# Kernel tuning notes

Measured on AMD Instinct MI355X. Metric: run time of the kernel, lower is better.

The kernel has to match this reference:

```python
import jax, jax.numpy as jnp
import numpy as np

DT = 1.0
S = 64            # num_sites
D = 2 * S         # state_dim
LOG_2PI = float(np.log(2.0 * np.pi))

def _selectors():
    s0 = np.zeros((2, 4), np.float32); s0[:, 0:2] = np.eye(2)
    s1 = np.zeros((2, 4), np.float32); s1[:, 2:4] = np.eye(2)
    cr = 0.5 * (s0 + s1)
    # [target=2, source=2, 2, 4]; off-diagonal pairs use the averaged selector
    return jnp.asarray(np.stack([np.stack([s0, cr]), np.stack([cr, s1])]))

SEL = _selectors()

def project_lon_lat(lon, lat):
    # lon, lat: [B,S]
    lat0 = lat.mean(-1, keepdims=True)
    lon0 = lon.mean(-1, keepdims=True)
    km = 111.32
    x = (lon - lon0) * (km * jnp.cos(jnp.deg2rad(lat0)))
    y = (lat - lat0) * km
    coords = jnp.stack([x, y], -1)                        # [B,S,2]
    h = coords[:, :, None, :] - coords[:, None, :, :]
    dist = jnp.sqrt((h ** 2).sum(-1) + 1e-12)
    npos = (dist > 1e-6).sum((-1, -2)).astype(coords.dtype)
    scale = dist.sum((-1, -2)) / jnp.maximum(npos, 1.0)
    return coords / jnp.maximum(scale, 1e-6)[:, None, None]

def build_A(h, mu, sigma, coupling, damping, eyeD):
    # h: [B,S,S,2], mu: [B,4], sigma: [B,4,4]
    B = mu.shape[0]
    sigma = 0.5 * (sigma + jnp.swapaxes(sigma, -1, -2))
    dm = jnp.einsum('tsab,nb->tsna', SEL, mu)                     # [2,2,B,2]
    dc = jnp.einsum('tsab,nbc,tsdc->tsnad', SEL, sigma, SEL)      # [2,2,B,2,2]
    dc = 0.5 * (dc + jnp.swapaxes(dc, -1, -2))
    eye2 = jnp.eye(2, dtype=h.dtype)
    Dm = (1.0 + 1e-4) * eye2 + (2.0 * DT ** 2) * dc
    Dinv = jnp.linalg.inv(Dm)
    _, logdet = jnp.linalg.slogdet(Dm)
    diff = h[None, None] - DT * dm[:, :, :, None, None, :]        # [2,2,B,S,S,2]
    q = jnp.einsum('tsbijd,tsbdf,tsbijf->tsbij', diff, Dinv, diff)
    ker = jnp.exp(-0.5 * (q + logdet[..., None, None]))
    ker = ker / jnp.maximum(ker.sum(-1, keepdims=True), 1e-6)
    ker = jnp.moveaxis(ker, 2, 0)                                 # [B,2,2,S,S]
    op = ker * coupling[None, :, :, None, None]
    op = jnp.transpose(op, (0, 1, 3, 2, 4)).reshape(B, D, D)
    return eyeD + DT * (op - damping * eyeD)

def _update(m, P, z_t, r2, eyeD):
    # Kalman measurement update with H = I, R = r2*I; returns per-sample NLL term
    Sm = P + r2 * eyeD
    v = z_t - m
    Sinv_v = jnp.linalg.solve(Sm, v[..., None])[..., 0]
    _, logdet = jnp.linalg.slogdet(Sm)
    nll_t = 0.5 * ((v * Sinv_v).sum(-1) + logdet + D * LOG_2PI)
    K = jnp.swapaxes(jnp.linalg.solve(Sm, P), -1, -2)   # P @ Sm^{-1} (P, Sm symmetric)
    m = m + jnp.einsum('bij,bj->bi', K, v)
    P = jnp.einsum('bij,bjk->bik', eyeD - K, P)
    return m, P, nll_t

def reference(z_seq, site_lon, site_lat, mu_seq, sigma_seq,
              log_q_proc, log_r_obs, log_p0, log_damping,
              init_mean, coupling_raw):
    B, T = z_seq.shape[0], z_seq.shape[1]
    z = z_seq.reshape(B, T, D)
    dtype = z.dtype
    eyeD = jnp.eye(D, dtype=dtype)
    r2 = jnp.exp(log_r_obs) ** 2
    q2 = jnp.exp(log_q_proc) ** 2
    damping = jnp.exp(log_damping)
    coupling = jnp.eye(2, dtype=dtype) + 0.25 * jnp.tanh(coupling_raw)

    lon = jnp.broadcast_to(site_lon[None], (B, S))
    lat = jnp.broadcast_to(site_lat[None], (B, S))
    coords = project_lon_lat(lon, lat)
    h = coords[:, :, None, :] - coords[:, None, :, :]   # [B,S,S,2]

    m0 = jnp.broadcast_to(init_mean[None], (B, D))
    P0 = jnp.broadcast_to(jnp.exp(log_p0) ** 2 * eyeD, (B, D, D))
    m, P, nll0 = _update(m0, P0, z[:, 0], r2, eyeD)

    def step(carry, xs):
        m, P = carry
        mu_t, sigma_t, z_t = xs
        A = build_A(h, mu_t, sigma_t, coupling, damping, eyeD)
        m = jnp.einsum('bij,bj->bi', A, m)
        P = jnp.einsum('bij,bjk,blk->bil', A, P, A) + q2 * eyeD
        m, P, nll_t = _update(m, P, z_t, r2, eyeD)
        return (m, P), nll_t

    xs = (jnp.swapaxes(mu_seq, 0, 1), jnp.swapaxes(sigma_seq, 0, 1),
          jnp.swapaxes(z[:, 1:], 0, 1))
    (_, _), nll_rest = jax.lax.scan(step, (m, P), xs)
    nll = nll0 + nll_rest.sum(0)   # [B]
    return nll.mean()

def setup_inputs() -> dict:
    key = jax.random.key(0)
    ks = jax.random.split(key, 5)
    B, T = 16, 128
    z_seq = jax.random.normal(ks[0], (B, T, S, 2), jnp.float32)
    site_lon = 10.0 + 0.5 * jax.random.uniform(ks[1], (S,), jnp.float32)
    site_lat = 55.0 + 0.5 * jax.random.uniform(ks[2], (S,), jnp.float32)
    mu_seq = 0.5 * jax.random.normal(ks[3], (B, T - 1, 4), jnp.float32)
    L = 0.2 * jax.random.normal(ks[4], (B, T - 1, 4, 4), jnp.float32)
    sigma_seq = jnp.einsum('btij,btkj->btik', L, L)   # PSD covariances
    return {
        'z_seq': z_seq, 'site_lon': site_lon, 'site_lat': site_lat,
        'mu_seq': mu_seq, 'sigma_seq': sigma_seq,
        'log_q_proc': jnp.float32(-2.0), 'log_r_obs': jnp.float32(-2.0),
        'log_p0': jnp.float32(0.0), 'log_damping': jnp.float32(0.0),
        'init_mean': jnp.zeros((D,), jnp.float32),
        'coupling_raw': jnp.zeros((2, 2), jnp.float32),
    }
```

## Files before the change

### kernel.cpp

```cpp
#include <hip/hip_runtime.h>
#include <math.h>


#define SQ 64
#define DQ 128
#define TQ 128
#define BQ 16
#define LDP 132
#define LDB 136
#define WFLOATS 17408
#define NTH 1024
#define LOG2PI 1.8378770664093454f

#define SMEM_FLOATS 35472

typedef __attribute__((ext_vector_type(8))) short bf16x8;
typedef __attribute__((ext_vector_type(4))) float f32x4;

__device__ __forceinline__ void lds_fence() {
  __asm__ volatile("s_waitcnt lgkmcnt(0)" ::: "memory");
}

__device__ __forceinline__ unsigned short f2bf(float f) {
  unsigned u = __float_as_uint(f);
  u += 0x7fffu + ((u >> 16) & 1u);
  return (unsigned short)(u >> 16);
}
__device__ __forceinline__ uint4 pack8(const float* v) {
  uint4 r;
  r.x = (unsigned)f2bf(v[0]) | ((unsigned)f2bf(v[1]) << 16);
  r.y = (unsigned)f2bf(v[2]) | ((unsigned)f2bf(v[3]) << 16);
  r.z = (unsigned)f2bf(v[4]) | ((unsigned)f2bf(v[5]) << 16);
  r.w = (unsigned)f2bf(v[6]) | ((unsigned)f2bf(v[7]) << 16);
  return r;
}

__device__ __forceinline__ float block_reduce_sum(float v, float* red) {
  #pragma unroll
  for (int off = 32; off > 0; off >>= 1) v += __shfl_down(v, off);
  const int tid = threadIdx.x;
  if ((tid & 63) == 0) red[tid >> 6] = v;
  __syncthreads();
  v = 0.0f;
  #pragma unroll
  for (int w = 0; w < NTH / 64; w++) v += red[w];
  __syncthreads();
  return v;
}

__device__ __forceinline__ void chol16_f(float* __restrict__ Wf,
                                         float* __restrict__ mdiag,
                                         int b0, int lane) {
  float a[16];
  if (lane < 16) {
    const float4* rp = (const float4*)(Wf + (b0 + lane) * LDP + b0);
    float4 q0 = rp[0], q1 = rp[1], q2v = rp[2], q3 = rp[3];
    a[0]=q0.x; a[1]=q0.y; a[2]=q0.z; a[3]=q0.w;
    a[4]=q1.x; a[5]=q1.y; a[6]=q1.z; a[7]=q1.w;
    a[8]=q2v.x; a[9]=q2v.y; a[10]=q2v.z; a[11]=q2v.w;
    a[12]=q3.x; a[13]=q3.y; a[14]=q3.z; a[15]=q3.w;
  } else {
    #pragma unroll
    for (int i = 0; i < 16; i++) a[i] = 1.0f;
  }
  float myrinv = 1.0f;
  #pragma unroll
  for (int j = 0; j < 16; j++) {
    float dj = __shfl(a[j], j);
    float rinv = rsqrtf(dj);
    float lij = a[j] * rinv;
    a[j] = lij;
    if (lane == j) myrinv = rinv;
    #pragma unroll
    for (int k = j + 1; k < 16; k++) {
      float lkj = __shfl(lij, k);
      a[k] = fmaf(-lij, lkj, a[k]);
    }
  }
  if (lane < 16) {
    float4* rp = (float4*)(Wf + (b0 + lane) * LDP + b0);
    rp[0] = make_float4(a[0], a[1], a[2], a[3]);
    rp[1] = make_float4(a[4], a[5], a[6], a[7]);
    rp[2] = make_float4(a[8], a[9], a[10], a[11]);
    rp[3] = make_float4(a[12], a[13], a[14], a[15]);
    mdiag[b0 + lane] = myrinv;
  }
}

__device__ __forceinline__ void trinv_chain2(float* __restrict__ Wf,
                                             const float* __restrict__ mdiag,
                                             int J, int pass, int lane,
                                             bool do1) {
  const int c16 = lane & 15;
  const int j16 = 4 * (lane >> 4) + pass;
  const int sh = lane & 48;
  if (do1) {
    float row[16];
    const float4* rp = (const float4*)(Wf + (J * 16 + c16) * LDP + J * 16);
    float4 a0 = rp[0], a1 = rp[1], a2 = rp[2], a3 = rp[3];
    row[0]=a0.x; row[1]=a0.y; row[2]=a0.z; row[3]=a0.w;
    row[4]=a1.x; row[5]=a1.y; row[6]=a1.z; row[7]=a1.w;
    row[8]=a2.x; row[9]=a2.y; row[10]=a2.z; row[11]=a2.w;
    row[12]=a3.x; row[13]=a3.y; row[14]=a3.z; row[15]=a3.w;
    float s = (c16 == j16) ? 1.0f : 0.0f;
    #pragma unroll
    for (int k = 0; k < 16; k++) {
      if (c16 == k) s *= mdiag[J * 16 + k];
      float sk = __shfl(s, sh | k);
      if (c16 > k) s = fmaf(-row[k], sk, s);
    }
    if (c16 > j16) Wf[(J * 16 + j16) * LDP + (J * 16 + c16)] = s;
    lds_fence();
  }
  const float md = mdiag[J * 16 + j16];
  const float* Mrow = Wf + (J * 16 + j16) * LDP + J * 16;
  #pragma unroll 1
  for (int I = J + 1; I < 8; I++) {
    const float* Lrow = Wf + (I * 16 + c16) * LDP + J * 16;
    float g = 0.0f;
    #pragma unroll
    for (int c4 = 0; c4 < 4; c4++) {
      float4 lv = *(const float4*)&Lrow[c4 * 4];
      float4 mq = *(const float4*)&Mrow[c4 * 4];
      float w0 = (c4*4+0 > j16) ? mq.x : ((c4*4+0 == j16) ? md : 0.0f);
      float w1 = (c4*4+1 > j16) ? mq.y : ((c4*4+1 == j16) ? md : 0.0f);
      float w2 = (c4*4+2 > j16) ? mq.z : ((c4*4+2 == j16) ? md : 0.0f);
      float w3 = (c4*4+3 > j16) ? mq.w : ((c4*4+3 == j16) ? md : 0.0f);
      g = fmaf(lv.x, w0, g); g = fmaf(lv.y, w1, g);
      g = fmaf(lv.z, w2, g); g = fmaf(lv.w, w3, g);
    }
    for (int K = J + 1; K < I; K++) {
      const float* LK = Lrow + (K - J) * 16;
      const float* MK = Wf + (J * 16 + j16) * LDP + K * 16;
      #pragma unroll
      for (int c4 = 0; c4 < 4; c4++) {
        float4 lv = *(const float4*)&LK[c4 * 4];
        float4 mq = *(const float4*)&MK[c4 * 4];
        g = fmaf(lv.x, mq.x, g); g = fmaf(lv.y, mq.y, g);
        g = fmaf(lv.z, mq.z, g); g = fmaf(lv.w, mq.w, g);
      }
    }
    if (I < 7) {
      float s = mdiag[I * 16 + c16] * g;
      #pragma unroll
      for (int k = 0; k < 15; k++) {
        float gk = __shfl(g, sh | k);
        if (k < c16) {
          float u = Wf[(I * 16 + k) * LDP + I * 16 + c16];
          s = fmaf(u, gk, s);
        }
      }
      Wf[(J * 16 + j16) * LDP + (I * 16 + c16)] = -s;
    } else {
      float row2[16];
      {
        const float4* rp2 = (const float4*)(Wf + (I * 16 + c16) * LDP + I * 16);
        float4 a0 = rp2[0], a1 = rp2[1], a2 = rp2[2], a3 = rp2[3];
        row2[0]=a0.x; row2[1]=a0.y; row2[2]=a0.z; row2[3]=a0.w;
        row2[4]=a1.x; row2[5]=a1.y; row2[6]=a1.z; row2[7]=a1.w;
        row2[8]=a2.x; row2[9]=a2.y; row2[10]=a2.z; row2[11]=a2.w;
        row2[12]=a3.x; row2[13]=a3.y; row2[14]=a3.z; row2[15]=a3.w;
      }
      float sv = g;
      #pragma unroll
      for (int k = 0; k < 16; k++) {
        if (c16 == k) sv *= mdiag[I * 16 + k];
        float sk = __shfl(sv, sh | k);
        if (c16 > k) sv = fmaf(-row2[k], sk, sv);
      }
      Wf[(J * 16 + j16) * LDP + (I * 16 + c16)] = -sv;
    }
    lds_fence();
  }
}

extern "C" __global__ __launch_bounds__(NTH, 4)
void ide_kf_kernel(const float* __restrict__ z_seq,
                   const float* __restrict__ site_lon,
                   const float* __restrict__ site_lat,
                   const float* __restrict__ mu_seq,
                   const float* __restrict__ sigma_seq,
                   const float* __restrict__ log_q,
                   const float* __restrict__ log_r,
                   const float* __restrict__ log_p0,
                   const float* __restrict__ log_damp,
                   const float* __restrict__ init_mean,
                   const float* __restrict__ coupling_raw,
                   float* __restrict__ ws) {
  extern __shared__ float smem[];
  float* Wf     = smem;
  float* B1f    = Wf + WFLOATS;
  float* B2f    = B1f + 8704;
  float* coords = B2f + 8704;
  float* mv     = coords + 128;
  float* vv     = mv + DQ;
  float* yv     = vv + DQ;
  float* mdiag  = yv + DQ;
  float* red    = mdiag + DQ;

  unsigned short* Tb  = (unsigned short*)Wf;
  unsigned short* Ab2 = (unsigned short*)Wf + 17408;
  unsigned short* Mtb = (unsigned short*)B1f;
  unsigned short* Pb  = (unsigned short*)B2f;
  unsigned short* Lhi = (unsigned short*)B1f;
  unsigned short* Llo = (unsigned short*)B2f;

  const int tid = threadIdx.x;
  const int lane = tid & 63;
  const int wave = tid >> 6;
  const int rb = wave >> 1, ch = wave & 1;
  const int m16 = lane & 15, quad = lane >> 4;
  const int grp = wave >> 2, pass = wave & 3;
  const int b = blockIdx.x;
  float* nll_out = ws;

  const float r2 = __expf(2.0f * log_r[0]);
  const float q2 = __expf(2.0f * log_q[0]);
  const float p0sq = __expf(2.0f * log_p0[0]);
  const float damping = __expf(log_damp[0]);
  const float cpl00 = 1.0f + 0.25f * tanhf(coupling_raw[0]);
  const float cpl01 = 0.25f * tanhf(coupling_raw[1]);
  const float cpl10 = 0.25f * tanhf(coupling_raw[2]);
  const float cpl11 = 1.0f + 0.25f * tanhf(coupling_raw[3]);

  float myLon = (tid < SQ) ? site_lon[tid] : 0.0f;
  float myLat = (tid < SQ) ? site_lat[tid] : 0.0f;
  float lat0 = block_reduce_sum(myLat, red) * (1.0f / 64.0f);
  float lon0 = block_reduce_sum(myLon, red) * (1.0f / 64.0f);
  if (tid < SQ) {
    const float km = 111.32f;
    float cs = cosf(lat0 * 0.017453292519943295f);
    coords[2 * tid]     = (myLon - lon0) * (km * cs);
    coords[2 * tid + 1] = (myLat - lat0) * km;
  }
  __syncthreads();
  float dsum = 0.0f, dcnt = 0.0f;
  for (int idx = tid; idx < SQ * SQ; idx += NTH) {
    int i = idx >> 6, j = idx & 63;
    float dx = coords[2 * i] - coords[2 * j];
    float dy = coords[2 * i + 1] - coords[2 * j + 1];
    float d = sqrtf(dx * dx + dy * dy + 1e-12f);
    dsum += d;
    if (d > 1e-6f) dcnt += 1.0f;
  }
  dsum = block_reduce_sum(dsum, red);
  dcnt = block_reduce_sum(dcnt, red);
  float scale = dsum / fmaxf(dcnt, 1.0f);
  float sdiv = 1.0f / fmaxf(scale, 1e-6f);
  if (tid < SQ) { coords[2 * tid] *= sdiv; coords[2 * tid + 1] *= sdiv; }

  for (int e = tid; e < WFLOATS / 4; e += NTH)
    ((float4*)Wf)[e] = make_float4(0.0f, 0.0f, 0.0f, 0.0f);
  for (int e = tid; e < 8704 / 4; e += NTH)
    ((float4*)B2f)[e] = make_float4(0.0f, 0.0f, 0.0f, 0.0f);
  __syncthreads();
  if (tid < DQ) {
    Wf[tid * LDP + tid] = p0sq + r2;
    mv[tid] = init_mean[tid];
  }
  __syncthreads();

  float nllp = 0.0f;

  #pragma unroll 1
  for (int t = 0; t < TQ; t++) {
    const float* zt = z_seq + ((size_t)b * TQ + t) * DQ;

    if (t > 0) {
      {
        f32x4 acc[4];
        #pragma unroll
        for (int c = 0; c < 4; c++) acc[c] = (f32x4){0.0f, 0.0f, 0.0f, 0.0f};
        #pragma unroll
        for (int ks = 0; ks < 4; ks++) {
          const int ko = 32 * ks + 8 * quad;
          bf16x8 a = *(const bf16x8*)(Ab2 + (16 * rb + m16) * LDB + ko);
          #pragma unroll
          for (int ct = 0; ct < 4; ct++) {
            bf16x8 bb = *(const bf16x8*)(Pb + (64 * ch + 16 * ct + m16) * LDB + ko);
            acc[ct] = __builtin_amdgcn_mfma_f32_16x16x32_bf16(a, bb, acc[ct], 0, 0, 0);
          }
        }
        #pragma unroll
        for (int ct = 0; ct < 4; ct++)
          #pragma unroll
          for (int reg = 0; reg < 4; reg++)
            Tb[(16 * rb + 4 * quad + reg) * LDB + 64 * ch + 16 * ct + m16] =
                f2bf(acc[ct][reg]);
        __syncthreads();
      }

      {
        const int ctmax = rb - 4 * ch;
        f32x4 acc[4];
        #pragma unroll
        for (int c = 0; c < 4; c++) acc[c] = (f32x4){0.0f, 0.0f, 0.0f, 0.0f};
        const bool gemv_wave = (wave == 1 || wave == 3);
        const int grow = (wave == 1) ? lane : 64 + lane;
        float newm = 0.0f;
        if (ctmax >= 0) {
          #pragma unroll
          for (int ks = 0; ks < 4; ks++) {
            const int ko = 32 * ks + 8 * quad;
            bf16x8 a = *(const bf16x8*)(Tb + (16 * rb + m16) * LDB + ko);
            #pragma unroll
            for (int ct = 0; ct < 4; ct++) {
              if (ct <= ctmax) {
                bf16x8 bb = *(const bf16x8*)(Ab2 + (64 * ch + 16 * ct + m16) * LDB + ko);
                acc[ct] = __builtin_amdgcn_mfma_f32_16x16x32_bf16(a, bb, acc[ct], 0, 0, 0);
              }
            }
          }
        } else if (gemv_wave) {
          const unsigned* ar = (const unsigned*)(Ab2 + grow * LDB);
          #pragma unroll 8
          for (int k2 = 0; k2 < 64; k2++) {
            unsigned p = ar[k2];
            newm = fmaf(__uint_as_float(p << 16), mv[2 * k2], newm);
            newm = fmaf(__uint_as_float(p & 0xffff0000u), mv[2 * k2 + 1], newm);
          }
        }
        __syncthreads();
        if (ctmax >= 0) {
          #pragma unroll
          for (int ct = 0; ct < 4; ct++) {
            if (ct <= ctmax) {
              #pragma unroll
              for (int reg = 0; reg < 4; reg++) {
                const int rg = 16 * rb + 4 * quad + reg;
                const int cgl = 64 * ch + 16 * ct + m16;
                Wf[rg * LDP + cgl] = acc[ct][reg] + ((rg == cgl) ? (q2 + r2) : 0.0f);
              }
            }
          }
        }
        if (gemv_wave) vv[grow] = zt[grow] - newm;
        if (wave == 0) {
          lds_fence();
          chol16_f(Wf, mdiag, 0, lane);
        }
        __syncthreads();
      }
    }

    if (t == 0) {
      if (tid < 64) {
        chol16_f(Wf, mdiag, 0, lane);
      } else if (tid < 192) {
        const int i = tid - 64;
        vv[i] = zt[i] - mv[i];
      }
      __syncthreads();
    }

    #pragma unroll 1
    for (int kb = 0; kb < 7; kb++) {
      const int b0k = kb * 16, base = b0k + 16, nbelow = DQ - base;
      if (tid < nbelow) {
        const int r = base + tid;
        float* wr = Wf + r * LDP + b0k;
        float w[16];
        #pragma unroll
        for (int u4 = 0; u4 < 4; u4++) {
          float4 w4 = *(const float4*)&wr[u4 * 4];
          w[u4*4] = w4.x; w[u4*4+1] = w4.y; w[u4*4+2] = w4.z; w[u4*4+3] = w4.w;
        }
        #pragma unroll
        for (int j = 0; j < 16; j++) {
          float s = w[j];
          #pragma unroll
          for (int l = 0; l < 16; l++) {
            if (l < j) s = fmaf(-w[l], Wf[(b0k + j) * LDP + b0k + l], s);
          }
          w[j] = s * mdiag[b0k + j];
        }
        #pragma unroll
        for (int u4 = 0; u4 < 4; u4++)
          *(float4*)&wr[u4 * 4] =
              make_float4(w[u4*4], w[u4*4+1], w[u4*4+2], w[u4*4+3]);
        unsigned short hs[16]; float lo[16];
        #pragma unroll
        for (int u = 0; u < 16; u++) {
          hs[u] = f2bf(w[u]);
          lo[u] = w[u] - __uint_as_float(((unsigned)hs[u]) << 16);
        }
        uint4 h0, h1;
        h0.x = hs[0] | ((unsigned)hs[1] << 16);   h0.y = hs[2] | ((unsigned)hs[3] << 16);
        h0.z = hs[4] | ((unsigned)hs[5] << 16);   h0.w = hs[6] | ((unsigned)hs[7] << 16);
        h1.x = hs[8] | ((unsigned)hs[9] << 16);   h1.y = hs[10] | ((unsigned)hs[11] << 16);
        h1.z = hs[12] | ((unsigned)hs[13] << 16); h1.w = hs[14] | ((unsigned)hs[15] << 16);
        unsigned short* hr = Lhi + r * LDB + b0k;
        unsigned short* lr = Llo + r * LDB + b0k;
        *(uint4*)(hr) = h0; *(uint4*)(hr + 8) = h1;
        *(uint4*)(lr) = pack8(lo); *(uint4*)(lr + 8) = pack8(lo + 8);
        const uint4 z4 = make_uint4(0u, 0u, 0u, 0u);
        *(uint4*)(hr + 16) = z4; *(uint4*)(hr + 24) = z4;
        *(uint4*)(lr + 16) = z4; *(uint4*)(lr + 24) = z4;
      }
      __syncthreads();
      if (wave <= 6 - kb) {
        const int bi = kb + 1 + wave;
        const int nch = (kb + 2) >> 1;
        f32x4 acc = (f32x4){0.0f, 0.0f, 0.0f, 0.0f};
        for (int c = 0; c < nch; c++) {
          const int ko = 32 * c + 8 * quad;
          bf16x8 ahi = *(const bf16x8*)(Lhi + (16 * bi + m16) * LDB + ko);
          bf16x8 alo = *(const bf16x8*)(Llo + (16 * bi + m16) * LDB + ko);
          bf16x8 bhi = *(const bf16x8*)(Lhi + (base + m16) * LDB + ko);
          bf16x8 blo = *(const bf16x8*)(Llo + (base + m16) * LDB + ko);
          acc = __builtin_amdgcn_mfma_f32_16x16x32_bf16(ahi, bhi, acc, 0, 0, 0);
          acc = __builtin_amdgcn_mfma_f32_16x16x32_bf16(ahi, blo, acc, 0, 0, 0);
          acc = __builtin_amdgcn_mfma_f32_16x16x32_bf16(alo, bhi, acc, 0, 0, 0);
        }
        #pragma unroll
        for (int reg = 0; reg < 4; reg++)
          Wf[(16 * bi + 4 * quad + reg) * LDP + base + m16] -= acc[reg];
        if (wave == 0) {
          lds_fence();
          chol16_f(Wf, mdiag, base, lane);
        }
      } else if (wave >= 8 && wave <= 11) {
        const int c16 = lane & 15;
        const int j16s = 4 * (lane >> 4) + (wave - 8);
        const int sh = lane & 48;
        float row[16];
        const float4* rp = (const float4*)(Wf + (b0k + c16) * LDP + b0k);
        float4 a0 = rp[0], a1 = rp[1], a2 = rp[2], a3 = rp[3];
        row[0]=a0.x; row[1]=a0.y; row[2]=a0.z; row[3]=a0.w;
        row[4]=a1.x; row[5]=a1.y; row[6]=a1.z; row[7]=a1.w;
        row[8]=a2.x; row[9]=a2.y; row[10]=a2.z; row[11]=a2.w;
        row[12]=a3.x; row[13]=a3.y; row[14]=a3.z; row[15]=a3.w;
        float s = (c16 == j16s) ? 1.0f : 0.0f;
        #pragma unroll
        for (int k = 0; k < 16; k++) {
          if (c16 == k) s *= mdiag[b0k + k];
          float sk = __shfl(s, sh | k);
          if (c16 > k) s = fmaf(-row[k], sk, s);
        }
        if (c16 > j16s) Wf[(b0k + j16s) * LDP + (b0k + c16)] = s;
      }
      __syncthreads();
    }

    {
      #pragma unroll 1
      for (int cc = 0; cc < 2; cc++) {
        const int J = cc ? (7 - grp) : grp;
        trinv_chain2(Wf, mdiag, J, pass, lane, cc == 1 && grp == 0);
      }
      __syncthreads();
    }

    {
      const int mrow = tid >> 3, kc = (tid & 7) * 16;
      float mtv[16];
      if (kc > mrow) {
        const float4* rp = (const float4*)(Wf + mrow * LDP + kc);
        float4 q0 = rp[0], q1 = rp[1], q2v = rp[2], q3 = rp[3];
        mtv[0]=q0.x; mtv[1]=q0.y; mtv[2]=q0.z; mtv[3]=q0.w;
        mtv[4]=q1.x; mtv[5]=q1.y; mtv[6]=q1.z; mtv[7]=q1.w;
        mtv[8]=q2v.x; mtv[9]=q2v.y; mtv[10]=q2v.z; mtv[11]=q2v.w;
        mtv[12]=q3.x; mtv[13]=q3.y; mtv[14]=q3.z; mtv[15]=q3.w;
      } else if (kc + 15 < mrow) {
        #pragma unroll
        for (int u = 0; u < 16; u++) mtv[u] = 0.0f;
      } else {
        #pragma unroll
        for (int u = 0; u < 16; u++) {
          const int k = kc + u;
          mtv[u] = (k > mrow) ? Wf[mrow * LDP + k]
                 : ((k == mrow) ? mdiag[mrow] : 0.0f);
        }
      }
      if (tid < DQ) {
        nllp -= __logf(mdiag[tid]);
        float s = mdiag[tid] * vv[tid];
        for (int k = 0; k < tid; k++) s = fmaf(Wf[k * LDP + tid], vv[k], s);
        yv[tid] = s;
      }
      unsigned short* mt = Mtb + mrow * LDB + kc;
      *(uint4*)(mt) = pack8(mtv);
      *(uint4*)(mt + 8) = pack8(mtv + 8);
      __syncthreads();
    }

    {
      f32x4 acc[4];
      #pragma unroll
      for (int c = 0; c < 4; c++) acc[c] = (f32x4){0.0f, 0.0f, 0.0f, 0.0f};
      if (tid < DQ) nllp += 0.5f * yv[tid] * yv[tid];
      const int ctmax = rb - 4 * ch;
      if (ctmax >= 0) {
        for (int ks = (rb >> 1); ks < 4; ks++) {
          const int ko = 32 * ks + 8 * quad;
          bf16x8 a = *(const bf16x8*)(Mtb + (16 * rb + m16) * LDB + ko);
          #pragma unroll
          for (int ct = 0; ct < 4; ct++) {
            if (ct <= ctmax) {
              bf16x8 bb = *(const bf16x8*)(Mtb + (64 * ch + 16 * ct + m16) * LDB + ko);
              acc[ct] = __builtin_amdgcn_mfma_f32_16x16x32_bf16(a, bb, acc[ct], 0, 0, 0);
            }
          }
        }
      }
      const float nr22 = -r2 * r2;
      #pragma unroll
      for (int ct = 0; ct < 4; ct++) {
        if (ct <= ctmax) {
          const bool strict = (ct < ctmax);
          #pragma unroll
          for (int reg = 0; reg < 4; reg++) {
            const int rg = 16 * rb + 4 * quad + reg;
            const int cgl = 64 * ch + 16 * ct + m16;
            unsigned short hv = f2bf(nr22 * acc[ct][reg] + ((rg == cgl) ? r2 : 0.0f));
            Pb[rg * LDB + cgl] = hv;
            if (strict) Pb[cgl * LDB + rg] = hv;
          }
        }
      }
      if (tid < DQ) {
        const unsigned* mr = (const unsigned*)(Mtb + tid * LDB);
        float s = 0.0f;
        #pragma unroll 8
        for (int k2 = 0; k2 < 64; k2++) {
          unsigned p = mr[k2];
          s = fmaf(__uint_as_float(p << 16), yv[2 * k2], s);
          s = fmaf(__uint_as_float(p & 0xffff0000u), yv[2 * k2 + 1], s);
        }
        mv[tid] = zt[tid] - r2 * s;
      }
      if (t < TQ - 1) {
        const float* mu_t = mu_seq + ((size_t)b * (TQ - 1) + t) * 4;
        const float* sg_t = sigma_seq + ((size_t)b * (TQ - 1) + t) * 16;
        const int unit = tid >> 2, q = tid & 3;
        const int r = unit >> 1, ss = unit & 1, tt = r >> 6, i = r & 63;
        float m0 = mu_t[0], m1 = mu_t[1], m2 = mu_t[2], m3 = mu_t[3];
        float dmx, dmy, c00, c01, c11;
        if (tt == 0 && ss == 0) {
          dmx = m0; dmy = m1;
          c00 = sg_t[0]; c01 = 0.5f * (sg_t[1] + sg_t[4]); c11 = sg_t[5];
        } else if (tt == 1 && ss == 1) {
          dmx = m2; dmy = m3;
          c00 = sg_t[10]; c01 = 0.5f * (sg_t[11] + sg_t[14]); c11 = sg_t[15];
        } else {
          dmx = 0.5f * (m0 + m2); dmy = 0.5f * (m1 + m3);
          float s00 = sg_t[0];
          float s02 = 0.5f * (sg_t[2] + sg_t[8]);
          float s22 = sg_t[10];
          float s01 = 0.5f * (sg_t[1] + sg_t[4]);
          float s03 = 0.5f * (sg_t[3] + sg_t[12]);
          float s21 = 0.5f * (sg_t[9] + sg_t[6]);
          float s23 = 0.5f * (sg_t[11] + sg_t[14]);
          float s11 = sg_t[5];
          float s13 = 0.5f * (sg_t[7] + sg_t[13]);
          float s33 = sg_t[15];
          c00 = 0.25f * (s00 + s02 + s02 + s22);
          c01 = 0.25f * (s01 + s03 + s21 + s23);
          c11 = 0.25f * (s11 + s13 + s13 + s33);
        }
        float D00 = 1.0001f + 2.0f * c00;
        float D01 = 2.0f * c01;
        float D11 = 1.0001f + 2.0f * c11;
        float det = D00 * D11 - D01 * D01;
        float dinv = 1.0f / det;
        float d00 = D11 * dinv, d01 = -D01 * dinv, d11 = D00 * dinv;
        float ldts = __logf(det);
        float cix = coords[2 * i], ciy = coords[2 * i + 1];
        const float* cj = coords + q * 32;
        float kv[16];
        float rsum = 0.0f;
        #pragma unroll
        for (int u = 0; u < 16; u++) {
          float dx = cix - cj[2 * u] - dmx;
          float dy = ciy - cj[2 * u + 1] - dmy;
          float qf = d00 * dx * dx + 2.0f * d01 * dx * dy + d11 * dy * dy;
          kv[u] = __expf(-0.5f * (qf + ldts));
          rsum += kv[u];
        }
        float rtot = rsum + __shfl_xor(rsum, 1);
        rtot += __shfl_xor(rtot, 2);
        float cv = (tt == 0) ? ((ss == 0) ? cpl00 : cpl01)
                             : ((ss == 0) ? cpl10 : cpl11);
        float norm = cv / fmaxf(rtot, 1e-6f);
        #pragma unroll
        for (int u = 0; u < 16; u++) kv[u] *= norm;
        if (ss == tt && ((i >> 4) == q)) kv[i & 15] += 1.0f - damping;
        unsigned short* arow = Ab2 + r * LDB + ss * 64 + q * 16;
        *(uint4*)(arow) = pack8(kv);
        *(uint4*)(arow + 8) = pack8(kv + 8);
      }
      __syncthreads();
    }
  }

  float total = block_reduce_sum(nllp, red);
  if (tid == 0)
    nll_out[b] = total + (float)TQ * 0.5f * (float)DQ * LOG2PI;
}

extern "C" __global__ void ide_finalize(const float* __restrict__ part,
                                        float* __restrict__ out) {
  if (threadIdx.x == 0) {
    float s = 0.0f;
    for (int i = 0; i < BQ; i++) s += part[i];
    out[0] = s * (1.0f / BQ);
  }
}

extern "C" void kernel_launch(void* const* d_in, const int* in_sizes, int n_in,
                              void* d_out, int out_size, void* d_ws, size_t ws_size,
                              hipStream_t stream) {
  (void)in_sizes; (void)n_in; (void)out_size; (void)ws_size;
  const float* z_seq        = (const float*)d_in[0];
  const float* site_lon     = (const float*)d_in[1];
  const float* site_lat     = (const float*)d_in[2];
  const float* mu_seq       = (const float*)d_in[3];
  const float* sigma_seq    = (const float*)d_in[4];
  const float* log_q        = (const float*)d_in[5];
  const float* log_r        = (const float*)d_in[6];
  const float* log_p0       = (const float*)d_in[7];
  const float* log_damp     = (const float*)d_in[8];
  const float* init_mean    = (const float*)d_in[9];
  const float* coupling_raw = (const float*)d_in[10];
  float* ws = (float*)d_ws;
  float* out = (float*)d_out;

  const size_t smem_bytes = (size_t)SMEM_FLOATS * sizeof(float);
  hipFuncSetAttribute((const void*)ide_kf_kernel,
                      hipFuncAttributeMaxDynamicSharedMemorySize,
                      (int)smem_bytes);

  hipLaunchKernelGGL(ide_kf_kernel, dim3(BQ), dim3(NTH), smem_bytes, stream,
                     z_seq, site_lon, site_lat, mu_seq, sigma_seq,
                     log_q, log_r, log_p0, log_damp, init_mean, coupling_raw,
                     ws);
  hipLaunchKernelGGL(ide_finalize, dim3(1), dim3(64), 0, stream, ws, out);
}
```

Measured before the change: 7.806 ms.

## Overlap triangular-inverse block steps with Cholesky panel and parallelize y solve

Splits the block triangular-inverse chain into a noinline step function. Idle waves run the inverse updates for already-factored column blocks during the Cholesky panel phase, so only the remaining blocks are processed after factorization, with the work rebalanced across groups. Separately, the serial per-thread dot product for yv (up to 128 terms on 128 threads) is replaced with a 1024-thread split into 16-term partial sums reduced by xor shuffles. This shortens the critical path but adds branch divergence, noinline call overhead, and possible register or LDS-timing hazards.

```diff
diff --git a/kernel.cpp b/kernel.cpp
--- a/kernel.cpp
+++ b/kernel.cpp
@@ -87,35 +87,16 @@
   }
 }
 
-__device__ __forceinline__ void trinv_chain2(float* __restrict__ Wf,
-                                             const float* __restrict__ mdiag,
-                                             int J, int pass, int lane,
-                                             bool do1) {
+__device__ __attribute__((noinline)) void trinv_steps(
+    float* __restrict__ Wf, const float* __restrict__ mdiag,
+    int J, int pass, int lane, int I0, int I1) {
   const int c16 = lane & 15;
   const int j16 = 4 * (lane >> 4) + pass;
   const int sh = lane & 48;
-  if (do1) {
-    float row[16];
-    const float4* rp = (const float4*)(Wf + (J * 16 + c16) * LDP + J * 16);
-    float4 a0 = rp[0], a1 = rp[1], a2 = rp[2], a3 = rp[3];
-    row[0]=a0.x; row[1]=a0.y; row[2]=a0.z; row[3]=a0.w;
-    row[4]=a1.x; row[5]=a1.y; row[6]=a1.z; row[7]=a1.w;
-    row[8]=a2.x; row[9]=a2.y; row[10]=a2.z; row[11]=a2.w;
-    row[12]=a3.x; row[13]=a3.y; row[14]=a3.z; row[15]=a3.w;
-    float s = (c16 == j16) ? 1.0f : 0.0f;
-    #pragma unroll
-    for (int k = 0; k < 16; k++) {
-      if (c16 == k) s *= mdiag[J * 16 + k];
-      float sk = __shfl(s, sh | k);
-      if (c16 > k) s = fmaf(-row[k], sk, s);
-    }
-    if (c16 > j16) Wf[(J * 16 + j16) * LDP + (J * 16 + c16)] = s;
-    lds_fence();
-  }
   const float md = mdiag[J * 16 + j16];
   const float* Mrow = Wf + (J * 16 + j16) * LDP + J * 16;
   #pragma unroll 1
-  for (int I = J + 1; I < 8; I++) {
+  for (int I = I0; I < I1; I++) {
     const float* Lrow = Wf + (I * 16 + c16) * LDP + J * 16;
     float g = 0.0f;
     #pragma unroll
@@ -396,6 +377,10 @@
         const uint4 z4 = make_uint4(0u, 0u, 0u, 0u);
         *(uint4*)(hr + 16) = z4; *(uint4*)(hr + 24) = z4;
         *(uint4*)(lr + 16) = z4; *(uint4*)(lr + 24) = z4;
+      } else if (wave >= 2 && wave <= 13) {
+        const int hJ = (wave - 2) >> 2;
+        if (kb >= hJ + 2)
+          trinv_steps(Wf, mdiag, hJ, (wave - 2) & 3, lane, kb - 1, kb);
       }
       __syncthreads();
       if (wave <= 6 - kb) {
@@ -443,10 +428,35 @@
     }
 
     {
-      #pragma unroll 1
-      for (int cc = 0; cc < 2; cc++) {
-        const int J = cc ? (7 - grp) : grp;
-        trinv_chain2(Wf, mdiag, J, pass, lane, cc == 1 && grp == 0);
+      if (grp == 0) {
+        trinv_steps(Wf, mdiag, 0, pass, lane, 6, 8);
+        trinv_steps(Wf, mdiag, 6, pass, lane, 7, 8);
+      } else if (grp == 1) {
+        trinv_steps(Wf, mdiag, 1, pass, lane, 6, 8);
+        trinv_steps(Wf, mdiag, 5, pass, lane, 6, 8);
+      } else if (grp == 2) {
+        trinv_steps(Wf, mdiag, 2, pass, lane, 6, 8);
+        trinv_steps(Wf, mdiag, 4, pass, lane, 5, 8);
+      } else {
+        trinv_steps(Wf, mdiag, 3, pass, lane, 4, 8);
+        const int c16 = lane & 15;
+        const int j16s = 4 * (lane >> 4) + pass;
+        const int sh = lane & 48;
+        float row[16];
+        const float4* rp = (const float4*)(Wf + (112 + c16) * LDP + 112);
+        float4 a0 = rp[0], a1 = rp[1], a2 = rp[2], a3 = rp[3];
+        row[0]=a0.x; row[1]=a0.y; row[2]=a0.z; row[3]=a0.w;
+        row[4]=a1.x; row[5]=a1.y; row[6]=a1.z; row[7]=a1.w;
+        row[8]=a2.x; row[9]=a2.y; row[10]=a2.z; row[11]=a2.w;
+        row[12]=a3.x; row[13]=a3.y; row[14]=a3.z; row[15]=a3.w;
+        float s = (c16 == j16s) ? 1.0f : 0.0f;
+        #pragma unroll
+        for (int k = 0; k < 16; k++) {
+          if (c16 == k) s *= mdiag[112 + k];
+          float sk = __shfl(s, sh | k);
+          if (c16 > k) s = fmaf(-row[k], sk, s);
+        }
+        if (c16 > j16s) Wf[(112 + j16s) * LDP + (112 + c16)] = s;
       }
       __syncthreads();
     }
@@ -472,11 +482,22 @@
                  : ((k == mrow) ? mdiag[mrow] : 0.0f);
         }
       }
-      if (tid < DQ) {
-        nllp -= __logf(mdiag[tid]);
-        float s = mdiag[tid] * vv[tid];
-        for (int k = 0; k < tid; k++) s = fmaf(Wf[k * LDP + tid], vv[k], s);
-        yv[tid] = s;
+      {
+        float p = 0.0f;
+        #pragma unroll
+        for (int u = 0; u < 16; u++) {
+          const int k = kc + u;
+          float val = (k < mrow) ? Wf[k * LDP + mrow]
+                    : ((k == mrow) ? mdiag[mrow] : 0.0f);
+          p = fmaf(val, vv[k], p);
+        }
+        p += __shfl_xor(p, 1);
+        p += __shfl_xor(p, 2);
+        p += __shfl_xor(p, 4);
+        if ((tid & 7) == 0) {
+          yv[mrow] = p;
+          nllp -= __logf(mdiag[mrow]);
+        }
       }
       unsigned short* mt = Mtb + mrow * LDB + kc;
       *(uint4*)(mt) = pack8(mtv);
```

After: 9.000 ms. +15.3%, slower.
